# Kernel tuning notes

Measured on AMD Instinct MI355X. Metric: run time of the kernel, lower is better.

## Reference

```python
import jax, jax.numpy as jnp
import numpy as np

B, C, H, W = 16, 512, 32, 32
CQ = C // 8  # 64
EPS = 1e-5


def _conv1x1(x, Wt, b=None):
    # x: (B,C,H,W), Wt: (O,C) -> (B,O,H,W)
    y = jnp.einsum('bchw,oc->bohw', x, Wt)
    if b is not None:
        y = y + b[None, :, None, None]
    return y


def setup_inputs() -> dict:
    key = jax.random.key(0)
    ks = jax.random.split(key, 12)
    s = 0.02
    return {
        'rgb':    jax.random.normal(ks[0], (B, C, H, W), jnp.float32),
        'depth':  jax.random.normal(ks[1], (B, C, H, W), jnp.float32),
        'Wq_rgb': jax.random.normal(ks[2], (CQ, C), jnp.float32) * s,
        'bq_rgb': jnp.zeros((CQ,), jnp.float32),
        'Wk_dep': jax.random.normal(ks[3], (CQ, C), jnp.float32) * s,
        'bk_dep': jnp.zeros((CQ,), jnp.float32),
        'Wv_dep': jax.random.normal(ks[4], (C, C), jnp.float32) * s,
        'bv_dep': jnp.zeros((C,), jnp.float32),
        'Wq_dep': jax.random.normal(ks[5], (CQ, C), jnp.float32) * s,
        'bq_dep': jnp.zeros((CQ,), jnp.float32),
        'Wk_rgb': jax.random.normal(ks[6], (CQ, C), jnp.float32) * s,
        'bk_rgb': jnp.zeros((CQ,), jnp.float32),
        'Wv_rgb': jax.random.normal(ks[7], (C, C), jnp.float32) * s,
        'bv_rgb': jnp.zeros((C,), jnp.float32),
        'W_fuse': jax.random.normal(ks[8], (C, 2 * C), jnp.float32) * s,
        'gamma':  jnp.ones((C,), jnp.float32),
        'beta':   jnp.zeros((C,), jnp.float32),
    }


def reference(rgb, depth, Wq_rgb, bq_rgb, Wk_dep, bk_dep, Wv_dep, bv_dep,
              Wq_dep, bq_dep, Wk_rgb, bk_rgb, Wv_rgb, bv_rgb, W_fuse, gamma, beta):
    b, c, h, w = rgb.shape
    hw = h * w
    scale = jnp.asarray(c, rgb.dtype) ** 0.5  # note: full C, as in source

    # RGB attends to depth
    q = _conv1x1(rgb, Wq_rgb, bq_rgb).reshape(b, -1, hw).transpose(0, 2, 1)   # (B,HW,CQ)
    k = _conv1x1(depth, Wk_dep, bk_dep).reshape(b, -1, hw)                    # (B,CQ,HW)
    v = _conv1x1(depth, Wv_dep, bv_dep).reshape(b, -1, hw).transpose(0, 2, 1) # (B,HW,C)
    attn = jax.nn.softmax(jnp.einsum('bnd,bdm->bnm', q, k) / scale, axis=-1)
    rgb_att = jnp.einsum('bnm,bmc->bnc', attn, v).transpose(0, 2, 1).reshape(b, c, h, w)

    # Depth attends to RGB
    q2 = _conv1x1(depth, Wq_dep, bq_dep).reshape(b, -1, hw).transpose(0, 2, 1)
    k2 = _conv1x1(rgb, Wk_rgb, bk_rgb).reshape(b, -1, hw)
    v2 = _conv1x1(rgb, Wv_rgb, bv_rgb).reshape(b, -1, hw).transpose(0, 2, 1)
    attn2 = jax.nn.softmax(jnp.einsum('bnd,bdm->bnm', q2, k2) / scale, axis=-1)
    dep_att = jnp.einsum('bnm,bmc->bnc', attn2, v2).transpose(0, 2, 1).reshape(b, c, h, w)

    cat = jnp.concatenate([rgb_att, dep_att], axis=1)      # (B,2C,H,W)
    fused = jnp.einsum('bchw,oc->bohw', cat, W_fuse)        # 1x1 conv, no bias

    # BatchNorm2d in training mode (batch statistics, biased variance)
    mean = fused.mean(axis=(0, 2, 3))
    var = fused.var(axis=(0, 2, 3))
    normed = (fused - mean[None, :, None, None]) * jax.lax.rsqrt(var + EPS)[None, :, None, None]
    out = normed * gamma[None, :, None, None] + beta[None, :, None, None]
    return jax.nn.relu(out)
```

## Files before the change

kernel.cpp:

```cpp
#include <hip/hip_runtime.h>
#include <math.h>

#define NB 16
#define CC 512
#define CQ 64
#define HWN 1024

typedef float4 f4;
typedef __bf16 bf16x8 __attribute__((ext_vector_type(8)));
typedef float f32x4 __attribute__((ext_vector_type(4)));
typedef __attribute__((ext_vector_type(8))) unsigned short ushort8v;

__device__ __forceinline__ unsigned short f2bf(float f) {
    unsigned int u = __float_as_uint(f);
    u = (u + 0x7fffu + ((u >> 16) & 1u)) >> 16;
    return (unsigned short)u;
}
__device__ __forceinline__ float bf2f(unsigned short u) {
    return __uint_as_float(((unsigned int)u) << 16);
}

__device__ __forceinline__ void gload16(const unsigned short* g, unsigned short* l) {
    __builtin_amdgcn_global_load_lds(
        (const __attribute__((address_space(1))) unsigned int*)g,
        (__attribute__((address_space(3))) unsigned int*)l,
        16, 0, 0);
}

template<int BM, int BN, int BIAS, bool OBF16, int ZSH, bool STATS>
__global__ __launch_bounds__(256)
void mfma_g(const unsigned short* __restrict__ A, long sAlo, long sAhi, int lda,
            const unsigned short* __restrict__ B, long sBlo, long sBhi, int ldb,
            const float* __restrict__ bias, long sBiasHi,
            void* __restrict__ Cout, long sClo, long sChi, int ldc,
            int Ksize, float alpha, float* __restrict__ statsAcc)
{
    constexpr int MF = BM / 32;
    constexpr int NF = BN / 32;
    constexpr int CA = BM / 32;
    constexpr int CB = BN / 32;
    __shared__ unsigned short As[2][BM * 64];
    __shared__ unsigned short Bs[2][BN * 64];

    const int gx = gridDim.x, gy = gridDim.y;
    int f = blockIdx.x + gx * (blockIdx.y + gy * blockIdx.z);
    const int nwg = gx * gy * gridDim.z;
    f = (f & 7) * (nwg >> 3) + (f >> 3);
    const int bx = f % gx; const int t2 = f / gx;
    const int by = t2 % gy; const int bz = t2 / gy;

    const int zlo = ZSH ? (bz & ((1 << ZSH) - 1)) : 0;
    const int zhi = bz >> ZSH;

    const int t = threadIdx.x, lane = t & 63, wid = t >> 6;
    const int wm = (wid >> 1) * (BM / 2), wn = (wid & 1) * (BN / 2);
    const int m0 = by * BM, n0 = bx * BN;
    const unsigned short* Ab = A + (long)zlo * sAlo + (long)zhi * sAhi;
    const unsigned short* Bb = B + (long)zlo * sBlo + (long)zhi * sBhi;

    const int srow = lane >> 3;
    const int scol = ((lane & 7) ^ srow) << 3;
    const unsigned short* gA[CA]; const unsigned short* gB[CB];
    unsigned short* lA[CA]; unsigned short* lB[CB];
#pragma unroll
    for (int c = 0; c < CA; ++c) {
        const int seg = wid + 4 * c;
        gA[c] = Ab + (long)(m0 + seg * 8 + srow) * lda + scol;
        lA[c] = &As[0][seg * 512];
    }
#pragma unroll
    for (int c = 0; c < CB; ++c) {
        const int seg = wid + 4 * c;
        gB[c] = Bb + (long)(n0 + seg * 8 + srow) * ldb + scol;
        lB[c] = &Bs[0][seg * 512];
    }

    f32x4 acc[MF][NF] = {};
    const int l15 = lane & 15, slot = lane >> 4;

#pragma unroll
    for (int c = 0; c < CA; ++c) gload16(gA[c], lA[c]);
#pragma unroll
    for (int c = 0; c < CB; ++c) gload16(gB[c], lB[c]);
    __syncthreads();

    const int nt = Ksize >> 6;
    int cur = 0;
    for (int tt = 0; tt < nt; ++tt) {
        if (tt + 1 < nt) {
            const int ko = (tt + 1) << 6;
            const int nb = cur ^ 1;
#pragma unroll
            for (int c = 0; c < CA; ++c) gload16(gA[c] + ko, lA[c] + nb * (BM * 64));
#pragma unroll
            for (int c = 0; c < CB; ++c) gload16(gB[c] + ko, lB[c] + nb * (BN * 64));
        }
        bf16x8 alo[MF], ahi[MF], blo[NF], bhi[NF];
#pragma unroll
        for (int i = 0; i < MF; ++i) {
            const int r = wm + i * 16 + l15;
            alo[i] = *(const bf16x8*)&As[cur][r * 64 + ((slot ^ (r & 7)) << 3)];
            ahi[i] = *(const bf16x8*)&As[cur][r * 64 + (((slot + 4) ^ (r & 7)) << 3)];
        }
#pragma unroll
        for (int j = 0; j < NF; ++j) {
            const int r = wn + j * 16 + l15;
            blo[j] = *(const bf16x8*)&Bs[cur][r * 64 + ((slot ^ (r & 7)) << 3)];
            bhi[j] = *(const bf16x8*)&Bs[cur][r * 64 + (((slot + 4) ^ (r & 7)) << 3)];
        }
#pragma unroll
        for (int i = 0; i < MF; ++i)
#pragma unroll
            for (int j = 0; j < NF; ++j) {
                acc[i][j] = __builtin_amdgcn_mfma_f32_16x16x32_bf16(alo[i], blo[j], acc[i][j], 0, 0, 0);
                acc[i][j] = __builtin_amdgcn_mfma_f32_16x16x32_bf16(ahi[i], bhi[j], acc[i][j], 0, 0, 0);
            }
        __syncthreads();
        cur ^= 1;
    }

    unsigned short* C16 = (unsigned short*)Cout + (long)zlo * sClo + (long)zhi * sChi;
    float*          C32 = (float*)Cout + (long)zlo * sClo + (long)zhi * sChi;
    const float* biasb = (BIAS != 0) ? bias + (long)zhi * sBiasHi : nullptr;
    const int r0 = slot << 2;
#pragma unroll
    for (int i = 0; i < MF; ++i) {
#pragma unroll
        for (int r = 0; r < 4; ++r) {
            const int m = m0 + wm + i * 16 + r0 + r;
            const float brow = (BIAS == 1) ? biasb[m] : 0.0f;
            float ps = 0.0f, ps2 = 0.0f;
#pragma unroll
            for (int j = 0; j < NF; ++j) {
                const int n = n0 + wn + j * 16 + l15;
                const float bb = (BIAS == 2) ? biasb[n] : brow;
                const float o = alpha * (acc[i][j][r] + bb);
                if (OBF16) C16[(long)m * ldc + n] = f2bf(o);
                else       C32[(long)m * ldc + n] = o;
                if (STATS) { ps += o; ps2 += o * o; }
            }
            if (STATS) {
#pragma unroll
                for (int off = 8; off; off >>= 1) {
                    ps  += __shfl_xor(ps, off);
                    ps2 += __shfl_xor(ps2, off);
                }
                if (l15 == 0) {
                    const int slot2 = ((zlo * gx + bx) << 1) + (wid & 1);
                    statsAcc[(long)m * 256 + slot2]          = ps;
                    statsAcc[131072 + (long)m * 256 + slot2] = ps2;
                }
            }
        }
    }
}

__global__ __launch_bounds__(256)
void attn_fused3(const unsigned short* __restrict__ QK, unsigned short* __restrict__ Pcat)
{
    __shared__ float ws16[16][4];
    const int t = threadIdx.x, lane = t & 63, w = t >> 6;
    const int bx = blockIdx.x, b = blockIdx.y, dir = blockIdx.z;
    const unsigned short* Q = QK + (long)(dir ? b : 16 + b) * 131072;
    const unsigned short* K = QK + (long)(dir ? 16 + b : b) * 131072 + 64;
    const int l15 = lane & 15, slot = lane >> 4, kg = slot << 3;

    const long mrow = (long)bx * 16 + l15;
    bf16x8 aq0 = *(const bf16x8*)&Q[mrow * 128 + kg];
    bf16x8 aq1 = *(const bf16x8*)&Q[mrow * 128 + 32 + kg];

    const int colbase = w << 8;
    const int rbase = slot << 2;
    f32x4 e[4][4];
    float rowp[4] = {0.0f, 0.0f, 0.0f, 0.0f};
#pragma unroll
    for (int c = 0; c < 4; ++c) {
        const int n0 = colbase + (c << 6);
        bf16x8 bk0[4], bk1[4];
#pragma unroll
        for (int j = 0; j < 4; ++j) {
            const long krow = n0 + (j << 4) + l15;
            bk0[j] = *(const bf16x8*)&K[krow * 128 + kg];
            bk1[j] = *(const bf16x8*)&K[krow * 128 + 32 + kg];
        }
#pragma unroll
        for (int j = 0; j < 4; ++j) {
            f32x4 a = {0.f, 0.f, 0.f, 0.f};
            a = __builtin_amdgcn_mfma_f32_16x16x32_bf16(aq0, bk0[j], a, 0, 0, 0);
            a = __builtin_amdgcn_mfma_f32_16x16x32_bf16(aq1, bk1[j], a, 0, 0, 0);
#pragma unroll
            for (int r = 0; r < 4; ++r) {
                const float ev = __expf(a[r]);
                e[c][j][r] = ev;
                rowp[r] += ev;
            }
        }
    }
#pragma unroll
    for (int off = 1; off < 16; off <<= 1) {
#pragma unroll
        for (int r = 0; r < 4; ++r) rowp[r] += __shfl_xor(rowp[r], off);
    }
    if (l15 == 0) {
#pragma unroll
        for (int r = 0; r < 4; ++r) ws16[rbase + r][w] = rowp[r];
    }
    __syncthreads();
    float inv[4];
#pragma unroll
    for (int r = 0; r < 4; ++r) {
        f4 s = *(const f4*)ws16[rbase + r];
        inv[r] = 1.0f / (s.x + s.y + s.z + s.w);
    }
    unsigned short* dstb = Pcat + ((long)(b * 1024 + bx * 16)) * 2048 + dir * 1024;
#pragma unroll
    for (int c = 0; c < 4; ++c) {
#pragma unroll
        for (int j = 0; j < 4; ++j) {
            const int col = colbase + (c << 6) + (j << 4) + l15;
#pragma unroll
            for (int r = 0; r < 4; ++r)
                dstb[(long)(rbase + r) * 2048 + col] = f2bf(e[c][j][r] * inv[r]);
        }
    }
}

__global__ __launch_bounds__(256)
void transpose_cvt2(const float* __restrict__ src_dep, const float* __restrict__ src_rgb,
                    unsigned short* __restrict__ dst)
{
    __shared__ float tile[64][65];
    const int t = threadIdx.x;
    const int z = blockIdx.z;
    const float* s = (z < 16 ? src_dep : src_rgb) + (long)(z & 15) * 524288;
    unsigned short* d = dst + (long)z * 524288;
    const int c0 = blockIdx.x << 6, r0 = blockIdx.y << 6;
    const int lr = t >> 4, lc = (t & 15) << 2;
#pragma unroll
    for (int i = 0; i < 4; ++i) {
        f4 v = *(const f4*)(s + (long)(r0 + lr + i * 16) * HWN + c0 + lc);
        *(f4*)&tile[lr + i * 16][lc] = v;
    }
    __syncthreads();
#pragma unroll
    for (int i = 0; i < 4; ++i) {
        const int crow = lr + i * 16;
        ushort4 o;
        o.x = f2bf(tile[lc + 0][crow]);
        o.y = f2bf(tile[lc + 1][crow]);
        o.z = f2bf(tile[lc + 2][crow]);
        o.w = f2bf(tile[lc + 3][crow]);
        *(ushort4*)&d[(long)(c0 + crow) * CC + r0 + lc] = o;
    }
}

__global__ __launch_bounds__(256)
void prep_all(const float* __restrict__ Wv_dep, const float* __restrict__ Wv_rgb,
              const float* __restrict__ W_fuse,
              const float* __restrict__ wqd, const float* __restrict__ wkd,
              const float* __restrict__ wqr, const float* __restrict__ wkr,
              const float* __restrict__ bqd, const float* __restrict__ bkd,
              const float* __restrict__ bqr, const float* __restrict__ bkr,
              const float* __restrict__ bvd, const float* __restrict__ bvr,
              unsigned short* __restrict__ WvT, unsigned short* __restrict__ Wfb,
              unsigned short* __restrict__ Wqk, float* __restrict__ bfuse,
              float* __restrict__ biascat, float s)
{
    __shared__ float tile[64][65];
    const int blk = blockIdx.x, t = threadIdx.x;

    if (blk < 128) {
        const int z = blk >> 6, tx = blk & 63;
        const float* src = z ? Wv_rgb : Wv_dep;
        unsigned short* d = WvT + (long)z * 262144;
        const int c0 = (tx & 7) << 6, r0 = (tx >> 3) << 6;
        const int lr = t >> 4, lc = (t & 15) << 2;
#pragma unroll
        for (int i = 0; i < 4; ++i) {
            f4 v = *(const f4*)(src + (long)(r0 + lr + i * 16) * CC + c0 + lc);
            *(f4*)&tile[lr + i * 16][lc] = v;
        }
        __syncthreads();
#pragma unroll
        for (int i = 0; i < 4; ++i) {
            const int crow = lr + i * 16;
            ushort4 o;
            o.x = f2bf(tile[lc + 0][crow]);
            o.y = f2bf(tile[lc + 1][crow]);
            o.z = f2bf(tile[lc + 2][crow]);
            o.w = f2bf(tile[lc + 3][crow]);
            *(ushort4*)&d[(long)(c0 + crow) * CC + r0 + lc] = o;
        }
    } else if (blk < 640) {
        const int i4 = (blk - 128) * 256 + t;
        f4 v = ((const f4*)W_fuse)[i4];
        ushort4 o;
        o.x = f2bf(v.x); o.y = f2bf(v.y); o.z = f2bf(v.z); o.w = f2bf(v.w);
        ((ushort4*)Wfb)[i4] = o;
    } else if (blk < 768) {
        const int i4 = (blk - 640) * 256 + t;
        const int row = i4 >> 7;
        const int seg = row >> 6;
        const float* src = (seg == 0) ? wqd : (seg == 1) ? wkd : (seg == 2) ? wqr : wkr;
        const float sc = (seg & 1) ? 1.0f : s;
        f4 v = ((const f4*)src)[((row & 63) << 7) + (i4 & 127)];
        ushort4 o;
        o.x = f2bf(v.x * sc); o.y = f2bf(v.y * sc);
        o.z = f2bf(v.z * sc); o.w = f2bf(v.w * sc);
        ((ushort4*)Wqk)[i4] = o;
    } else if (blk < 1280) {
        const int o = blk - 768;
        const float* row = W_fuse + (long)o * 1024;
        float sum = row[t] * bvd[t] + row[512 + t] * bvr[t]
                  + row[256 + t] * bvd[256 + t] + row[768 + t] * bvr[256 + t];
#pragma unroll
        for (int off = 32; off; off >>= 1) sum += __shfl_xor(sum, off);
        float* red = &tile[0][0];
        if ((t & 63) == 0) red[t >> 6] = sum;
        __syncthreads();
        if (t == 0) bfuse[o] = red[0] + red[1] + red[2] + red[3];
    } else {
        float v;
        if (t < 64)       v = bqd[t] * s;
        else if (t < 128) v = bkd[t - 64];
        else if (t < 192) v = bqr[t - 128] * s;
        else              v = bkr[t - 192];
        biascat[t] = v;
    }
}

__global__ __launch_bounds__(256)
void bn_finalize(const float* __restrict__ part, float* __restrict__ stats)
{
    const int c = blockIdx.x, t = threadIdx.x;
    float s1 = part[(long)c * 256 + t];
    float s2 = part[131072 + (long)c * 256 + t];
#pragma unroll
    for (int off = 32; off; off >>= 1) {
        s1 += __shfl_xor(s1, off);
        s2 += __shfl_xor(s2, off);
    }
    __shared__ float r1[4], r2[4];
    if ((t & 63) == 0) { r1[t >> 6] = s1; r2[t >> 6] = s2; }
    __syncthreads();
    if (t == 0) {
        const float S1 = r1[0] + r1[1] + r1[2] + r1[3];
        const float S2 = r2[0] + r2[1] + r2[2] + r2[3];
        const float mean = S1 * (1.0f / 16384.0f);
        const float var  = S2 * (1.0f / 16384.0f) - mean * mean;
        stats[c]      = mean;
        stats[CC + c] = rsqrtf(var + 1e-5f);
    }
}

__global__ __launch_bounds__(256)
void bn_apply_bf16(const unsigned short* __restrict__ fused, const float* __restrict__ stats,
                   const float* __restrict__ gamma, const float* __restrict__ beta,
                   float* __restrict__ out)
{
    const long i8 = (long)blockIdx.x * 256 + threadIdx.x;
    ushort8v v = ((const ushort8v*)fused)[i8];
    const int o = (int)((i8 >> 7) & 511);
    const float is = stats[CC + o];
    const float g  = gamma[o] * is;
    const float bb = beta[o] - stats[o] * g;
    f4 o0, o1;
    o0.x = fmaxf(fmaf(bf2f(v[0]), g, bb), 0.0f);
    o0.y = fmaxf(fmaf(bf2f(v[1]), g, bb), 0.0f);
    o0.z = fmaxf(fmaf(bf2f(v[2]), g, bb), 0.0f);
    o0.w = fmaxf(fmaf(bf2f(v[3]), g, bb), 0.0f);
    o1.x = fmaxf(fmaf(bf2f(v[4]), g, bb), 0.0f);
    o1.y = fmaxf(fmaf(bf2f(v[5]), g, bb), 0.0f);
    o1.z = fmaxf(fmaf(bf2f(v[6]), g, bb), 0.0f);
    o1.w = fmaxf(fmaf(bf2f(v[7]), g, bb), 0.0f);
    ((f4*)out)[i8 * 2]     = o0;
    ((f4*)out)[i8 * 2 + 1] = o1;
}

static constexpr long B_depT  = 0;
static constexpr long B_rgbT  = 16777216;
static constexpr long B_WvT1  = 33554432;
static constexpr long B_Wfb   = 34603008;
static constexpr long B_Wqk   = 35651584;
static constexpr long B_Wc1   = 35913728;
static constexpr long B_bfu   = 36962304;
static constexpr long B_bias  = 36964352;
static constexpr long B_QK    = 36966400;
static constexpr long B_Acat  = 45355008;
static constexpr long B_Pcat  = 78909440;
static constexpr long B_fused = 146018304;
static constexpr long B_stats = 179572736;
static constexpr long B_part  = 179576832;

extern "C" void kernel_launch(void* const* d_in, const int* in_sizes, int n_in,
                              void* d_out, int out_size, void* d_ws, size_t ws_size,
                              hipStream_t stream)
{
    const float* rgb    = (const float*)d_in[0];
    const float* depth  = (const float*)d_in[1];
    const float* Wq_rgb = (const float*)d_in[2];
    const float* bq_rgb = (const float*)d_in[3];
    const float* Wk_dep = (const float*)d_in[4];
    const float* bk_dep = (const float*)d_in[5];
    const float* Wv_dep = (const float*)d_in[6];
    const float* bv_dep = (const float*)d_in[7];
    const float* Wq_dep = (const float*)d_in[8];
    const float* bq_dep = (const float*)d_in[9];
    const float* Wk_rgb = (const float*)d_in[10];
    const float* bk_rgb = (const float*)d_in[11];
    const float* Wv_rgb = (const float*)d_in[12];
    const float* bv_rgb = (const float*)d_in[13];
    const float* W_fuse = (const float*)d_in[14];
    const float* gamma  = (const float*)d_in[15];
    const float* beta   = (const float*)d_in[16];
    char* ws = (char*)d_ws;
    float* out = (float*)d_out;

    const float inv_scale = 0.044194173824159223f;
    dim3 blk(256);

    unsigned short* depT = (unsigned short*)(ws + B_depT);
    unsigned short* WvT1 = (unsigned short*)(ws + B_WvT1);
    unsigned short* Wfb  = (unsigned short*)(ws + B_Wfb);
    unsigned short* Wqk  = (unsigned short*)(ws + B_Wqk);
    unsigned short* Wc1  = (unsigned short*)(ws + B_Wc1);
    float*          bfu  = (float*)(ws + B_bfu);
    float*          bias = (float*)(ws + B_bias);
    unsigned short* QK   = (unsigned short*)(ws + B_QK);
    unsigned short* Acat = (unsigned short*)(ws + B_Acat);
    unsigned short* Pcat = (unsigned short*)(ws + B_Pcat);
    unsigned short* fused= (unsigned short*)(ws + B_fused);
    float*          stats= (float*)(ws + B_stats);
    float*          part = (float*)(ws + B_part);

    transpose_cvt2<<<dim3(16, 8, 32), blk, 0, stream>>>(depth, rgb, depT);
    prep_all<<<1281, blk, 0, stream>>>(Wv_dep, Wv_rgb, W_fuse,
        Wq_dep, Wk_dep, Wq_rgb, Wk_rgb, bq_dep, bk_dep, bq_rgb, bk_rgb,
        bv_dep, bv_rgb, WvT1, Wfb, Wqk, bfu, bias, inv_scale);

    mfma_g<128, 128, 0, true, 0, false><<<dim3(4, 4, 2), blk, 0, stream>>>(
        Wfb, 0, 512, 1024, WvT1, 0, 262144, 512, nullptr, 0,
        Wc1, 0, 262144, 512, 512, 1.0f, nullptr);

    mfma_g<128, 128, 2, true, 4, false><<<dim3(1, 8, 32), blk, 0, stream>>>(
        depT, 524288, 8388608, 512, Wqk, 0, 65536, 512, bias, 128,
        QK, 131072, 2097152, 128, 512, 1.0f, nullptr);

    mfma_g<128, 128, 0, true, 4, false><<<dim3(8, 4, 32), blk, 0, stream>>>(
        Wc1, 0, 262144, 512, depT, 524288, 8388608, 512, nullptr, 0,
        Acat, 1048576, 1024, 2048, 512, 1.0f, nullptr);

    attn_fused3<<<dim3(64, NB, 2), blk, 0, stream>>>(QK, Pcat);

    mfma_g<128, 128, 1, true, 4, true><<<dim3(8, 4, 16), blk, 0, stream>>>(
        Acat, 1048576, 0, 2048, Pcat, 2097152, 0, 2048, bfu, 0,
        fused, 524288, 0, 1024, 2048, 1.0f, part);

    bn_finalize<<<512, blk, 0, stream>>>(part, stats);
    bn_apply_bf16<<<4096, blk, 0, stream>>>(fused, stats, gamma, beta, out);
}
```

Measured before the change: 171.1 us.

## Add BK template for GEMM tiles, shrink QK tile, fuse BN finalize into apply

Makes the MFMA GEMM's K-tile depth a template parameter, with a BK=32 path that uses a matching LDS swizzle. The QK projection now runs with a 64x128 tile and BK=32 on twice as many workgroups, and the V-projection GEMM uses BK=32. Both aim to lower LDS use and raise occupancy. The separate BN finalize kernel is removed: each apply block now reduces the partial sums for its two channels itself. This saves a launch and the stats round-trip, but every block redoes the reduction redundantly.

```diff
diff --git a/kernel.cpp b/kernel.cpp
--- a/kernel.cpp
+++ b/kernel.cpp
@@ -27,7 +27,7 @@
         16, 0, 0);
 }
 
-template<int BM, int BN, int BIAS, bool OBF16, int ZSH, bool STATS>
+template<int BM, int BN, int BK, int BIAS, bool OBF16, int ZSH, bool STATS>
 __global__ __launch_bounds__(256)
 void mfma_g(const unsigned short* __restrict__ A, long sAlo, long sAhi, int lda,
             const unsigned short* __restrict__ B, long sBlo, long sBhi, int ldb,
@@ -35,12 +35,15 @@
             void* __restrict__ Cout, long sClo, long sChi, int ldc,
             int Ksize, float alpha, float* __restrict__ statsAcc)
 {
-    constexpr int MF = BM / 32;
-    constexpr int NF = BN / 32;
-    constexpr int CA = BM / 32;
-    constexpr int CB = BN / 32;
-    __shared__ unsigned short As[2][BM * 64];
-    __shared__ unsigned short Bs[2][BN * 64];
+    constexpr int MF  = BM / 32;
+    constexpr int NF  = BN / 32;
+    constexpr int LPR = BK / 8;
+    constexpr int RPG = 64 / LPR;
+    constexpr int CA  = BM / RPG / 4;
+    constexpr int CB  = BN / RPG / 4;
+    constexpr int SWM = LPR - 1;
+    __shared__ unsigned short As[2][BM * BK];
+    __shared__ unsigned short Bs[2][BN * BK];
 
     const int gx = gridDim.x, gy = gridDim.y;
     int f = blockIdx.x + gx * (blockIdx.y + gy * blockIdx.z);
@@ -58,25 +61,26 @@
     const unsigned short* Ab = A + (long)zlo * sAlo + (long)zhi * sAhi;
     const unsigned short* Bb = B + (long)zlo * sBlo + (long)zhi * sBhi;
 
-    const int srow = lane >> 3;
-    const int scol = ((lane & 7) ^ srow) << 3;
+    const int srow = lane / LPR;
+    const int slt  = lane & SWM;
+    const int scol = ((slt ^ (srow & SWM)) << 3);
     const unsigned short* gA[CA]; const unsigned short* gB[CB];
     unsigned short* lA[CA]; unsigned short* lB[CB];
 #pragma unroll
     for (int c = 0; c < CA; ++c) {
         const int seg = wid + 4 * c;
-        gA[c] = Ab + (long)(m0 + seg * 8 + srow) * lda + scol;
+        gA[c] = Ab + (long)(m0 + seg * RPG + srow) * lda + scol;
         lA[c] = &As[0][seg * 512];
     }
 #pragma unroll
     for (int c = 0; c < CB; ++c) {
         const int seg = wid + 4 * c;
-        gB[c] = Bb + (long)(n0 + seg * 8 + srow) * ldb + scol;
+        gB[c] = Bb + (long)(n0 + seg * RPG + srow) * ldb + scol;
         lB[c] = &Bs[0][seg * 512];
     }
 
     f32x4 acc[MF][NF] = {};
-    const int l15 = lane & 15, slot = lane >> 4;
+    const int l15 = lane & 15, q = lane >> 4;
 
 #pragma unroll
     for (int c = 0; c < CA; ++c) gload16(gA[c], lA[c]);
@@ -84,37 +88,56 @@
     for (int c = 0; c < CB; ++c) gload16(gB[c], lB[c]);
     __syncthreads();
 
-    const int nt = Ksize >> 6;
+    const int nt = Ksize / BK;
     int cur = 0;
     for (int tt = 0; tt < nt; ++tt) {
         if (tt + 1 < nt) {
-            const int ko = (tt + 1) << 6;
+            const int ko = (tt + 1) * BK;
             const int nb = cur ^ 1;
 #pragma unroll
-            for (int c = 0; c < CA; ++c) gload16(gA[c] + ko, lA[c] + nb * (BM * 64));
-#pragma unroll
-            for (int c = 0; c < CB; ++c) gload16(gB[c] + ko, lB[c] + nb * (BN * 64));
-        }
-        bf16x8 alo[MF], ahi[MF], blo[NF], bhi[NF];
-#pragma unroll
-        for (int i = 0; i < MF; ++i) {
-            const int r = wm + i * 16 + l15;
-            alo[i] = *(const bf16x8*)&As[cur][r * 64 + ((slot ^ (r & 7)) << 3)];
-            ahi[i] = *(const bf16x8*)&As[cur][r * 64 + (((slot + 4) ^ (r & 7)) << 3)];
-        }
-#pragma unroll
-        for (int j = 0; j < NF; ++j) {
-            const int r = wn + j * 16 + l15;
-            blo[j] = *(const bf16x8*)&Bs[cur][r * 64 + ((slot ^ (r & 7)) << 3)];
-            bhi[j] = *(const bf16x8*)&Bs[cur][r * 64 + (((slot + 4) ^ (r & 7)) << 3)];
-        }
-#pragma unroll
-        for (int i = 0; i < MF; ++i)
+            for (int c = 0; c < CA; ++c) gload16(gA[c] + ko, lA[c] + nb * (BM * BK));
+#pragma unroll
+            for (int c = 0; c < CB; ++c) gload16(gB[c] + ko, lB[c] + nb * (BN * BK));
+        }
+        if (BK == 64) {
+            bf16x8 alo[MF], ahi[MF], blo[NF], bhi[NF];
+#pragma unroll
+            for (int i = 0; i < MF; ++i) {
+                const int r = wm + i * 16 + l15;
+                alo[i] = *(const bf16x8*)&As[cur][r * 64 + ((q ^ (r & 7)) << 3)];
+                ahi[i] = *(const bf16x8*)&As[cur][r * 64 + (((q + 4) ^ (r & 7)) << 3)];
+            }
 #pragma unroll
             for (int j = 0; j < NF; ++j) {
-                acc[i][j] = __builtin_amdgcn_mfma_f32_16x16x32_bf16(alo[i], blo[j], acc[i][j], 0, 0, 0);
-                acc[i][j] = __builtin_amdgcn_mfma_f32_16x16x32_bf16(ahi[i], bhi[j], acc[i][j], 0, 0, 0);
-            }
+                const int r = wn + j * 16 + l15;
+                blo[j] = *(const bf16x8*)&Bs[cur][r * 64 + ((q ^ (r & 7)) << 3)];
+                bhi[j] = *(const bf16x8*)&Bs[cur][r * 64 + (((q + 4) ^ (r & 7)) << 3)];
+            }
+#pragma unroll
+            for (int i = 0; i < MF; ++i)
+#pragma unroll
+                for (int j = 0; j < NF; ++j) {
+                    acc[i][j] = __builtin_amdgcn_mfma_f32_16x16x32_bf16(alo[i], blo[j], acc[i][j], 0, 0, 0);
+                    acc[i][j] = __builtin_amdgcn_mfma_f32_16x16x32_bf16(ahi[i], bhi[j], acc[i][j], 0, 0, 0);
+                }
+        } else {
+            bf16x8 av[MF], bv[NF];
+#pragma unroll
+            for (int i = 0; i < MF; ++i) {
+                const int r = wm + i * 16 + l15;
+                av[i] = *(const bf16x8*)&As[cur][r * 32 + ((q ^ (r & 3)) << 3)];
+            }
+#pragma unroll
+            for (int j = 0; j < NF; ++j) {
+                const int r = wn + j * 16 + l15;
+                bv[j] = *(const bf16x8*)&Bs[cur][r * 32 + ((q ^ (r & 3)) << 3)];
+            }
+#pragma unroll
+            for (int i = 0; i < MF; ++i)
+#pragma unroll
+                for (int j = 0; j < NF; ++j)
+                    acc[i][j] = __builtin_amdgcn_mfma_f32_16x16x32_bf16(av[i], bv[j], acc[i][j], 0, 0, 0);
+        }
         __syncthreads();
         cur ^= 1;
     }
@@ -122,7 +145,7 @@
     unsigned short* C16 = (unsigned short*)Cout + (long)zlo * sClo + (long)zhi * sChi;
     float*          C32 = (float*)Cout + (long)zlo * sClo + (long)zhi * sChi;
     const float* biasb = (BIAS != 0) ? bias + (long)zhi * sBiasHi : nullptr;
-    const int r0 = slot << 2;
+    const int r0 = q << 2;
 #pragma unroll
     for (int i = 0; i < MF; ++i) {
 #pragma unroll
@@ -330,40 +353,43 @@
 }
 
 __global__ __launch_bounds__(256)
-void bn_finalize(const float* __restrict__ part, float* __restrict__ stats)
-{
-    const int c = blockIdx.x, t = threadIdx.x;
-    float s1 = part[(long)c * 256 + t];
-    float s2 = part[131072 + (long)c * 256 + t];
+void bn_apply_f(const unsigned short* __restrict__ fused, const float* __restrict__ part,
+                const float* __restrict__ gamma, const float* __restrict__ beta,
+                float* __restrict__ out)
+{
+    __shared__ float red[4][4];
+    const int t = threadIdx.x, blk = blockIdx.x;
+    const int c0 = (blk * 2) & 511, c1 = c0 + 1;
+    float a = part[(long)c0 * 256 + t];
+    float b = part[131072 + (long)c0 * 256 + t];
+    float c = part[(long)c1 * 256 + t];
+    float d = part[131072 + (long)c1 * 256 + t];
 #pragma unroll
     for (int off = 32; off; off >>= 1) {
-        s1 += __shfl_xor(s1, off);
-        s2 += __shfl_xor(s2, off);
-    }
-    __shared__ float r1[4], r2[4];
-    if ((t & 63) == 0) { r1[t >> 6] = s1; r2[t >> 6] = s2; }
+        a += __shfl_xor(a, off); b += __shfl_xor(b, off);
+        c += __shfl_xor(c, off); d += __shfl_xor(d, off);
+    }
+    if ((t & 63) == 0) {
+        const int w = t >> 6;
+        red[0][w] = a; red[1][w] = b; red[2][w] = c; red[3][w] = d;
+    }
     __syncthreads();
-    if (t == 0) {
-        const float S1 = r1[0] + r1[1] + r1[2] + r1[3];
-        const float S2 = r2[0] + r2[1] + r2[2] + r2[3];
-        const float mean = S1 * (1.0f / 16384.0f);
-        const float var  = S2 * (1.0f / 16384.0f) - mean * mean;
-        stats[c]      = mean;
-        stats[CC + c] = rsqrtf(var + 1e-5f);
-    }
-}
-
-__global__ __launch_bounds__(256)
-void bn_apply_bf16(const unsigned short* __restrict__ fused, const float* __restrict__ stats,
-                   const float* __restrict__ gamma, const float* __restrict__ beta,
-                   float* __restrict__ out)
-{
-    const long i8 = (long)blockIdx.x * 256 + threadIdx.x;
+    const float S1a = red[0][0] + red[0][1] + red[0][2] + red[0][3];
+    const float S2a = red[1][0] + red[1][1] + red[1][2] + red[1][3];
+    const float S1b = red[2][0] + red[2][1] + red[2][2] + red[2][3];
+    const float S2b = red[3][0] + red[3][1] + red[3][2] + red[3][3];
+    const float mean0 = S1a * (1.0f / 16384.0f);
+    const float is0   = rsqrtf(S2a * (1.0f / 16384.0f) - mean0 * mean0 + 1e-5f);
+    const float mean1 = S1b * (1.0f / 16384.0f);
+    const float is1   = rsqrtf(S2b * (1.0f / 16384.0f) - mean1 * mean1 + 1e-5f);
+
+    const long i8 = (long)blk * 256 + t;
+    const int  oc = (t >> 7) ? c1 : c0;
+    const float mean = (t >> 7) ? mean1 : mean0;
+    const float is   = (t >> 7) ? is1 : is0;
     ushort8v v = ((const ushort8v*)fused)[i8];
-    const int o = (int)((i8 >> 7) & 511);
-    const float is = stats[CC + o];
-    const float g  = gamma[o] * is;
-    const float bb = beta[o] - stats[o] * g;
+    const float g  = gamma[oc] * is;
+    const float bb = beta[oc] - mean * g;
     f4 o0, o1;
     o0.x = fmaxf(fmaf(bf2f(v[0]), g, bb), 0.0f);
     o0.y = fmaxf(fmaf(bf2f(v[1]), g, bb), 0.0f);
@@ -389,7 +415,6 @@
 static constexpr long B_Acat  = 45355008;
 static constexpr long B_Pcat  = 78909440;
 static constexpr long B_fused = 146018304;
-static constexpr long B_stats = 179572736;
 static constexpr long B_part  = 179576832;
 
 extern "C" void kernel_launch(void* const* d_in, const int* in_sizes, int n_in,
@@ -430,7 +455,6 @@
     unsigned short* Acat = (unsigned short*)(ws + B_Acat);
     unsigned short* Pcat = (unsigned short*)(ws + B_Pcat);
     unsigned short* fused= (unsigned short*)(ws + B_fused);
-    float*          stats= (float*)(ws + B_stats);
     float*          part = (float*)(ws + B_part);
 
     transpose_cvt2<<<dim3(16, 8, 32), blk, 0, stream>>>(depth, rgb, depT);
@@ -438,24 +462,23 @@
         Wq_dep, Wk_dep, Wq_rgb, Wk_rgb, bq_dep, bk_dep, bq_rgb, bk_rgb,
         bv_dep, bv_rgb, WvT1, Wfb, Wqk, bfu, bias, inv_scale);
 
-    mfma_g<128, 128, 0, true, 0, false><<<dim3(4, 4, 2), blk, 0, stream>>>(
+    mfma_g<128, 128, 64, 0, true, 0, false><<<dim3(4, 4, 2), blk, 0, stream>>>(
         Wfb, 0, 512, 1024, WvT1, 0, 262144, 512, nullptr, 0,
         Wc1, 0, 262144, 512, 512, 1.0f, nullptr);
 
-    mfma_g<128, 128, 2, true, 4, false><<<dim3(1, 8, 32), blk, 0, stream>>>(
+    mfma_g<64, 128, 32, 2, true, 4, false><<<dim3(1, 16, 32), blk, 0, stream>>>(
         depT, 524288, 8388608, 512, Wqk, 0, 65536, 512, bias, 128,
         QK, 131072, 2097152, 128, 512, 1.0f, nullptr);
 
-    mfma_g<128, 128, 0, true, 4, false><<<dim3(8, 4, 32), blk, 0, stream>>>(
+    mfma_g<128, 128, 32, 0, true, 4, false><<<dim3(8, 4, 32), blk, 0, stream>>>(
         Wc1, 0, 262144, 512, depT, 524288, 8388608, 512, nullptr, 0,
         Acat, 1048576, 1024, 2048, 512, 1.0f, nullptr);
 
     attn_fused3<<<dim3(64, NB, 2), blk, 0, stream>>>(QK, Pcat);
 
-    mfma_g<128, 128, 1, true, 4, true><<<dim3(8, 4, 16), blk, 0, stream>>>(
+    mfma_g<128, 128, 64, 1, true, 4, true><<<dim3(8, 4, 16), blk, 0, stream>>>(
         Acat, 1048576, 0, 2048, Pcat, 2097152, 0, 2048, bfu, 0,
         fused, 524288, 0, 1024, 2048, 1.0f, part);
 
-    bn_finalize<<<512, blk, 0, stream>>>(part, stats);
-    bn_apply_bf16<<<4096, blk, 0, stream>>>(fused, stats, gamma, beta, out);
-}
+    bn_apply_f<<<4096, blk, 0, stream>>>(fused, part, gamma, beta, out);
+}
```

New measurement: 168.5 us. About the same (-1.5%).
